# Kernel optimization log

Hardware: AMD Instinct MI355X
Metric: run time of the kernel (lower is better)

## Reference

```python
import jax, jax.numpy as jnp
import numpy as np

# Sinabs LIF semantics (norm_input=True default):
#   v[t] = alpha * v[t-1] + (1 - alpha) * x[t],  alpha = exp(-1/tau_mem)
#   spikes = MultiSpike: max(floor(v / threshold), 0)   (default sa.ActivationFunction)
#   reset  = MembraneSubtract: v -= spikes * threshold
# threshold_low=None -> no lower clamp.

TAU_MEM = 20.0
THRESHOLD = 1.0
GRAD_WIDTH = 0.5   # sinabs SingleExponential surrogate defaults
GRAD_SCALE = 1.0

@jax.custom_vjp
def spike_fn(v):
    # MultiSpike: number of threshold crossings this step
    return jnp.maximum(jnp.floor(v / THRESHOLD), 0.0)

def _spike_fwd(v):
    return spike_fn(v), v

def _spike_bwd(v, g):
    # single-exponential surrogate gradient around threshold
    sg = (GRAD_SCALE / GRAD_WIDTH) * jnp.exp(-jnp.abs(v - THRESHOLD) / GRAD_WIDTH)
    return (g * sg,)

spike_fn.defvjp(_spike_fwd, _spike_bwd)

def lif_layer(x):
    # x: [B, T, N] synaptic input; returns spikes [B, T, N]
    alpha = jnp.exp(jnp.asarray(-1.0 / TAU_MEM, dtype=x.dtype))
    one_m = 1.0 - alpha

    def step(v, xt):
        v = alpha * v + one_m * xt
        s = spike_fn(v)
        v = v - s * THRESHOLD  # membrane subtract reset
        return v, s

    v0 = jnp.zeros(x.shape[:1] + x.shape[2:], dtype=x.dtype)  # [B, N]
    _, spikes = jax.lax.scan(step, v0, jnp.swapaxes(x, 0, 1))  # scan over T
    return jnp.swapaxes(spikes, 0, 1)

def setup_inputs() -> dict:
    key = jax.random.key(0)
    k0, k1, k2, k3 = jax.random.split(key, 4)
    B, T, C_IN = 256, 4096, 16
    data = jax.random.normal(k0, (B, T, C_IN), dtype=jnp.float32)
    # nn.Linear(in, out, bias=False) weights are [out, in], kaiming-uniform-ish scale
    w1 = jax.random.normal(k1, (16, 16), dtype=jnp.float32) / np.sqrt(16)
    w2 = jax.random.normal(k2, (32, 16), dtype=jnp.float32) / np.sqrt(16)
    w3 = jax.random.normal(k3, (10, 32), dtype=jnp.float32) / np.sqrt(32)
    return {"data": data, "w1": w1, "w2": w2, "w3": w3}

def reference(data, w1, w2, w3):
    out = jnp.einsum('btc,oc->bto', data, w1)
    out = lif_layer(out)
    out = jnp.einsum('btc,oc->bto', out, w2)
    out = lif_layer(out)
    out = jnp.einsum('btc,oc->bto', out, w3)
    out = lif_layer(out)
    return out
```

## Files before the change

kernel.cpp:

```cpp
#include <hip/hip_runtime.h>
#include <stdint.h>
#include <math.h>

#define T_STEPS 4096
#define BATCH   256
#define NB_BLK  256

__device__ __forceinline__ float lif_step(float& v, float xs, float alpha) {
    float vp = fmaf(alpha, v, xs);
    float fr = vp - floorf(vp);
    float vn = fminf(vp, fr);
    float s  = vp - vn;
    v = vn;
    return s;
}

__device__ __forceinline__ float ubf(uint32_t w, int k) {
    return (float)((w >> (k * 8)) & 0xffu);
}

__device__ __forceinline__ float dot16(const float wr[16],
    float4 c0, float4 c1, float4 c2, float4 c3)
{
    float p0 = fmaf(wr[1], c0.y, wr[0] * c0.x);
    p0 = fmaf(wr[2], c0.z, p0);  p0 = fmaf(wr[3], c0.w, p0);
    float p1 = fmaf(wr[5], c1.y, wr[4] * c1.x);
    p1 = fmaf(wr[6], c1.z, p1);  p1 = fmaf(wr[7], c1.w, p1);
    float p2 = fmaf(wr[9], c2.y, wr[8] * c2.x);
    p2 = fmaf(wr[10], c2.z, p2); p2 = fmaf(wr[11], c2.w, p2);
    float p3 = fmaf(wr[13], c3.y, wr[12] * c3.x);
    p3 = fmaf(wr[14], c3.z, p3); p3 = fmaf(wr[15], c3.w, p3);
    return (p0 + p1) + (p2 + p3);
}

__global__ __launch_bounds__(1024) void fused(
    const float* __restrict__ x, const float* __restrict__ w1,
    const float* __restrict__ w2, const float* __restrict__ w3,
    float* __restrict__ out, uint8_t* __restrict__ s1t,
    uint8_t* __restrict__ s2t,
    float alpha, float one_m, float alpha16)
{
    const int tid = threadIdx.x;
    const int b   = blockIdx.x;

    __shared__ __align__(16) float xbuf[16640];
    __shared__ float   sh_end[NB_BLK][16];
    __shared__ float   sh_m0[NB_BLK][16];
    __shared__ float   sh_m1[NB_BLK][16];
    __shared__ uint8_t sh_badseg[16][NB_BLK];
    __shared__ uint8_t sh_bm1[NB_BLK];
    __shared__ uint8_t sh_bm2[NB_BLK];
    __shared__ int     sh_badch, sh_spike, sh_flag2;

    const int co = tid & 15;
    const int sg = tid >> 4;
    const int wv = tid >> 6;
    const int ln = tid & 63;

    const float* xb = x + (size_t)b * T_STEPS * 16;
    const float4* xq4 = (const float4*)xb;

    float4 stg[4];
#pragma unroll
    for (int q = 0; q < 4; ++q)
        stg[q] = xq4[(wv * 4 + q) * 64 + ln];

    if (tid < 64)        ((uint32_t*)sh_bm1)[tid] = 0u;
    else if (tid < 128)  ((uint32_t*)sh_bm2)[tid - 64] = 0u;
    else if (tid == 128) { sh_badch = 0; sh_spike = 0; sh_flag2 = 0; }

    float4* o4 = (float4*)(out + (size_t)b * T_STEPS * 10);
    float4 z4 = make_float4(0.f, 0.f, 0.f, 0.f);
#pragma unroll
    for (int i = 0; i < 10; ++i) o4[i * 1024 + tid] = z4;

    float wr[16];
#pragma unroll
    for (int i = 0; i < 16; ++i) wr[i] = one_m * w1[co * 16 + i];

    const int sbase = sg * 260;
    const int wbase = (wv * 4) * 260 + ln * 4;

#pragma unroll
    for (int q = 0; q < 4; ++q)
        *(float4*)&xbuf[wbase + q * 260] = stg[q];

#pragma unroll
    for (int k = 0; k < 4; ++k) {
        if (k < 3) {
#pragma unroll
            for (int q = 0; q < 4; ++q)
                stg[q] = xq4[((k + 1) * 64 + wv * 4 + q) * 64 + ln];
        }

        float acc = 0.0f, m0 = -1e30f, m1 = -1e30f, pw = alpha;
#pragma unroll
        for (int j = 0; j < 16; ++j) {
            const float* rp = &xbuf[sbase + j * 16];
            float4 c0 = *(const float4*)(rp + 0);
            float4 c1 = *(const float4*)(rp + 4);
            float4 c2 = *(const float4*)(rp + 8);
            float4 c3 = *(const float4*)(rp + 12);
            float y = dot16(wr, c0, c1, c2, c3);
            acc = fmaf(alpha, acc, y);
            m0  = fmaxf(m0, acc);
            m1  = fmaxf(m1, acc + pw);
            pw *= alpha;
        }
        const int gs = k * 64 + sg;
        sh_end[gs][co] = acc;
        sh_m0[gs][co]  = m0;
        sh_m1[gs][co]  = m1;

        if (k < 3) {
#pragma unroll
            for (int q = 0; q < 4; ++q)
                *(float4*)&xbuf[wbase + q * 260] = stg[q];
        }
    }
    __syncthreads();

    if (tid < 16) {
        const int c = tid;
        float vs = 0.0f;
        int bad = 0;
#pragma unroll 8
        for (int s = 0; s < NB_BLK; ++s) {
            float vsu = fminf(fmaxf(vs + 1e-3f, 0.0f), 1.0f);
            float bound = fmaf(1.0f - vsu, sh_m0[s][c], vsu * sh_m1[s][c]);
            int sb = (bound >= 0.999f) ? 1 : 0;
            sh_badseg[c][s] = (uint8_t)sb;
            bad |= sb;
            vs = fmaf(alpha16, vs, sh_end[s][c]);
        }
        if (bad) atomicOr(&sh_badch, 1 << c);
    }
    __syncthreads();

    const int badmask = sh_badch;
    if (badmask) {
        uint4* sz = (uint4*)(s1t + (size_t)b * 16 * T_STEPS);
#pragma unroll
        for (int i = 0; i < 4; ++i) sz[i * 1024 + tid] = make_uint4(0u,0u,0u,0u);
        __syncthreads();

        int m = badmask;
        for (int i = 0; i < wv; ++i) m &= m - 1;
        if (ln == 0 && m) {
            const int c = __ffs(m) - 1;
            float wc[16];
#pragma unroll
            for (int i = 0; i < 16; ++i) wc[i] = one_m * w1[c * 16 + i];
            uint8_t* op = s1t + ((size_t)b * 16 + c) * T_STEPS;
            float v = 0.0f;
            int any = 0;
            for (int s = 0; s < NB_BLK; ++s) {
                if (!sh_badseg[c][s]) {
                    v = fmaf(alpha16, v, sh_end[s][c]);
                } else {
                    const float4* xr = (const float4*)xb + (size_t)s * 64;
                    uint32_t w[4] = {0u,0u,0u,0u};
#pragma unroll 4
                    for (int j = 0; j < 16; ++j) {
                        float y  = dot16(wc, xr[j*4+0], xr[j*4+1],
                                              xr[j*4+2], xr[j*4+3]);
                        float sp = lif_step(v, y, alpha);
                        w[j >> 2] |= ((uint32_t)(int)sp) << ((j & 3) * 8);
                    }
                    if (w[0] | w[1] | w[2] | w[3]) {
                        *(uint4*)(op + s * 16) = make_uint4(w[0], w[1], w[2], w[3]);
                        sh_bm1[s] = 1;
                        any = 1;
                    }
                }
            }
            if (any) sh_spike = 1;
        }
    }
    __syncthreads();

    if (sh_spike) {
        if (tid < 32) {
            const int c2 = tid;
            float wr2[16];
#pragma unroll
            for (int i = 0; i < 16; ++i) wr2[i] = one_m * w2[c2 * 16 + i];
            const uint8_t* sb1 = s1t + (size_t)b * 16 * T_STEPS;
            uint4* op2 = (uint4*)(s2t + ((size_t)b * 32 + c2) * T_STEPS);
            const uint4* bmv = (const uint4*)sh_bm1;
            uint8_t* bm2p = sh_bm2;
            float v = 0.0f;
            for (int sb = 0; sb < 16; ++sb) {
                uint4 bm = bmv[sb];
                if ((bm.x | bm.y | bm.z | bm.w) == 0u) {
                    if (v != 0.0f) {
                        for (int blk = 0; blk < 16 && v != 0.0f; ++blk) {
#pragma unroll
                            for (int j = 0; j < 16; ++j) v *= alpha;
                        }
                    }
                    continue;
                }
                for (int blk = 0; blk < 16; ++blk) {
                    uint32_t d = (blk < 4) ? bm.x : (blk < 8) ? bm.y
                               : (blk < 12) ? bm.z : bm.w;
                    uint32_t byte = (d >> ((blk & 3) * 8)) & 0xffu;
                    if (byte == 0u) {
                        if (v != 0.0f) {
#pragma unroll
                            for (int j = 0; j < 16; ++j) v *= alpha;
                        }
                        continue;
                    }
                    const int tb = sb * 16 + blk;
                    const int t0 = tb * 16;
                    uint4 S[16];
#pragma unroll
                    for (int c = 0; c < 16; ++c)
                        S[c] = *(const uint4*)(sb1 + (size_t)c * T_STEPS + t0);
                    uint32_t w[4] = {0u, 0u, 0u, 0u};
#pragma unroll
                    for (int j = 0; j < 16; ++j) {
                        float xv[16];
#pragma unroll
                        for (int c = 0; c < 16; ++c) {
                            uint32_t dd = (j < 4) ? S[c].x : (j < 8) ? S[c].y
                                        : (j < 12) ? S[c].z : S[c].w;
                            xv[c] = ubf(dd, j & 3);
                        }
                        float p0 = fmaf(wr2[1], xv[1], wr2[0] * xv[0]);
                        p0 = fmaf(wr2[2], xv[2], p0);   p0 = fmaf(wr2[3], xv[3], p0);
                        float p1 = fmaf(wr2[5], xv[5], wr2[4] * xv[4]);
                        p1 = fmaf(wr2[6], xv[6], p1);   p1 = fmaf(wr2[7], xv[7], p1);
                        float p2 = fmaf(wr2[9], xv[9], wr2[8] * xv[8]);
                        p2 = fmaf(wr2[10], xv[10], p2); p2 = fmaf(wr2[11], xv[11], p2);
                        float p3 = fmaf(wr2[13], xv[13], wr2[12] * xv[12]);
                        p3 = fmaf(wr2[14], xv[14], p3); p3 = fmaf(wr2[15], xv[15], p3);
                        float xs = (p0 + p1) + (p2 + p3);
                        float s = lif_step(v, xs, alpha);
                        w[j >> 2] |= ((uint32_t)(int)s) << ((j & 3) * 8);
                    }
                    op2[tb] = make_uint4(w[0], w[1], w[2], w[3]);
                    if (w[0] | w[1] | w[2] | w[3]) { bm2p[tb] = 1; sh_flag2 = 1; }
                }
            }
        }
        __syncthreads();

        if (sh_flag2 && tid < 16) {
            const int c3 = tid;
            const bool active = (c3 < 10);
            float wr3[32];
#pragma unroll
            for (int i = 0; i < 32; ++i)
                wr3[i] = active ? (one_m * w3[c3 * 32 + i]) : 0.0f;
            const uint8_t* sb2 = s2t + (size_t)b * 32 * T_STEPS;
            const uint4* bmv2 = (const uint4*)sh_bm2;
            float* ob = out + (size_t)b * T_STEPS * 10 + c3;
            float v = 0.0f;
            for (int sb = 0; sb < 16; ++sb) {
                uint4 bm = bmv2[sb];
                if ((bm.x | bm.y | bm.z | bm.w) == 0u) {
                    if (v != 0.0f) {
                        for (int blk = 0; blk < 16 && v != 0.0f; ++blk) {
#pragma unroll
                            for (int j = 0; j < 16; ++j) v *= alpha;
                        }
                    }
                    continue;
                }
                for (int blk = 0; blk < 16; ++blk) {
                    uint32_t d = (blk < 4) ? bm.x : (blk < 8) ? bm.y
                               : (blk < 12) ? bm.z : bm.w;
                    uint32_t byte = (d >> ((blk & 3) * 8)) & 0xffu;
                    if (byte == 0u) {
                        if (v != 0.0f) {
#pragma unroll
                            for (int j = 0; j < 16; ++j) v *= alpha;
                        }
                        continue;
                    }
                    const int t0 = (sb * 16 + blk) * 16;
                    uint4 S[32];
#pragma unroll
                    for (int c = 0; c < 32; ++c)
                        S[c] = *(const uint4*)(sb2 + (size_t)c * T_STEPS + t0);
#pragma unroll
                    for (int j = 0; j < 16; ++j) {
                        float xv[32];
#pragma unroll
                        for (int c = 0; c < 32; ++c) {
                            uint32_t dd = (j < 4) ? S[c].x : (j < 8) ? S[c].y
                                        : (j < 12) ? S[c].z : S[c].w;
                            xv[c] = ubf(dd, j & 3);
                        }
                        float p0 = fmaf(wr3[1], xv[1], wr3[0] * xv[0]);
                        p0 = fmaf(wr3[2],  xv[2],  p0); p0 = fmaf(wr3[3],  xv[3],  p0);
                        p0 = fmaf(wr3[4],  xv[4],  p0); p0 = fmaf(wr3[5],  xv[5],  p0);
                        p0 = fmaf(wr3[6],  xv[6],  p0); p0 = fmaf(wr3[7],  xv[7],  p0);
                        float p1 = fmaf(wr3[9], xv[9], wr3[8] * xv[8]);
                        p1 = fmaf(wr3[10], xv[10], p1); p1 = fmaf(wr3[11], xv[11], p1);
                        p1 = fmaf(wr3[12], xv[12], p1); p1 = fmaf(wr3[13], xv[13], p1);
                        p1 = fmaf(wr3[14], xv[14], p1); p1 = fmaf(wr3[15], xv[15], p1);
                        float p2 = fmaf(wr3[17], xv[17], wr3[16] * xv[16]);
                        p2 = fmaf(wr3[18], xv[18], p2); p2 = fmaf(wr3[19], xv[19], p2);
                        p2 = fmaf(wr3[20], xv[20], p2); p2 = fmaf(wr3[21], xv[21], p2);
                        p2 = fmaf(wr3[22], xv[22], p2); p2 = fmaf(wr3[23], xv[23], p2);
                        float p3 = fmaf(wr3[25], xv[25], wr3[24] * xv[24]);
                        p3 = fmaf(wr3[26], xv[26], p3); p3 = fmaf(wr3[27], xv[27], p3);
                        p3 = fmaf(wr3[28], xv[28], p3); p3 = fmaf(wr3[29], xv[29], p3);
                        p3 = fmaf(wr3[30], xv[30], p3); p3 = fmaf(wr3[31], xv[31], p3);
                        float xs = (p0 + p1) + (p2 + p3);
                        float s = lif_step(v, xs, alpha);
                        if (active && s != 0.0f) ob[(size_t)(t0 + j) * 10] = s;
                    }
                }
            }
        }
    }
}

extern "C" void kernel_launch(void* const* d_in, const int* in_sizes, int n_in,
                              void* d_out, int out_size, void* d_ws, size_t ws_size,
                              hipStream_t stream)
{
    const float* data = (const float*)d_in[0];
    const float* w1   = (const float*)d_in[1];
    const float* w2   = (const float*)d_in[2];
    const float* w3   = (const float*)d_in[3];
    float* out = (float*)d_out;

    uint8_t* ws  = (uint8_t*)d_ws;
    uint8_t* s1t = ws;
    uint8_t* s2t = ws + (16u << 20);

    const float alpha   = expf(-1.0f / 20.0f);
    const float one_m   = 1.0f - alpha;
    const float alpha16 = expf(-16.0f / 20.0f);

    fused<<<BATCH, 1024, 0, stream>>>(data, w1, w2, w3, out, s1t, s2t,
                                      alpha, one_m, alpha16);
}
```

Baseline: 165.2 us.

## Certify layer-1 quiescence per 4-step segment with per-thread register loads

Layer-1 screening now works on 4-step segments instead of 16-step blocks. Each thread loads its own 64 floats straight into registers, computes all 16 channels and packs fp16 max bounds with the end value into shared memory. This replaces the staged LDS buffer and shared-memory transposes. The serial certification scan is split across 8 groups per channel, each warmed up over 40 previous segments, and bad segments are kept as bitmasks. The finer granularity means fewer steps get recomputed exactly, but fp16 bounds and the truncated warm-up could misjudge a segment near the threshold.

```diff
diff --git a/kernel.cpp b/kernel.cpp
--- a/kernel.cpp
+++ b/kernel.cpp
@@ -1,10 +1,13 @@
 #include <hip/hip_runtime.h>
+#include <hip/hip_fp16.h>
 #include <stdint.h>
 #include <math.h>
 
 #define T_STEPS 4096
 #define BATCH   256
 #define NB_BLK  256
+#define NSEG    1024
+#define EPITCH  1025
 
 __device__ __forceinline__ float lif_step(float& v, float xs, float alpha) {
     float vp = fmaf(alpha, v, xs);
@@ -33,37 +36,30 @@
     return (p0 + p1) + (p2 + p3);
 }
 
-__global__ __launch_bounds__(1024) void fused(
+__global__ __launch_bounds__(1024, 4) void fused(
     const float* __restrict__ x, const float* __restrict__ w1,
     const float* __restrict__ w2, const float* __restrict__ w3,
     float* __restrict__ out, uint8_t* __restrict__ s1t,
     uint8_t* __restrict__ s2t,
-    float alpha, float one_m, float alpha16)
+    float alpha, float one_m, float alpha4)
 {
     const int tid = threadIdx.x;
     const int b   = blockIdx.x;
-
-    __shared__ __align__(16) float xbuf[16640];
-    __shared__ float   sh_end[NB_BLK][16];
-    __shared__ float   sh_m0[NB_BLK][16];
-    __shared__ float   sh_m1[NB_BLK][16];
-    __shared__ uint8_t sh_badseg[16][NB_BLK];
-    __shared__ uint8_t sh_bm1[NB_BLK];
-    __shared__ uint8_t sh_bm2[NB_BLK];
-    __shared__ int     sh_badch, sh_spike, sh_flag2;
-
-    const int co = tid & 15;
-    const int sg = tid >> 4;
-    const int wv = tid >> 6;
-    const int ln = tid & 63;
+    const int wv  = tid >> 6;
+    const int ln  = tid & 63;
+
+    __shared__ float2   sh_cert[16][EPITCH];
+    __shared__ uint32_t sh_badseg[16][NSEG / 32];
+    __shared__ uint8_t  sh_bm1[NB_BLK];
+    __shared__ uint8_t  sh_bm2[NB_BLK];
+    __shared__ int      sh_badch, sh_spike, sh_flag2;
 
     const float* xb = x + (size_t)b * T_STEPS * 16;
     const float4* xq4 = (const float4*)xb;
 
-    float4 stg[4];
-#pragma unroll
-    for (int q = 0; q < 4; ++q)
-        stg[q] = xq4[(wv * 4 + q) * 64 + ln];
+    float4 xr[16];
+#pragma unroll
+    for (int q = 0; q < 16; ++q) xr[q] = xq4[tid * 16 + q];
 
     if (tid < 64)        ((uint32_t*)sh_bm1)[tid] = 0u;
     else if (tid < 128)  ((uint32_t*)sh_bm2)[tid - 64] = 0u;
@@ -74,64 +70,50 @@
 #pragma unroll
     for (int i = 0; i < 10; ++i) o4[i * 1024 + tid] = z4;
 
-    float wr[16];
-#pragma unroll
-    for (int i = 0; i < 16; ++i) wr[i] = one_m * w1[co * 16 + i];
-
-    const int sbase = sg * 260;
-    const int wbase = (wv * 4) * 260 + ln * 4;
-
-#pragma unroll
-    for (int q = 0; q < 4; ++q)
-        *(float4*)&xbuf[wbase + q * 260] = stg[q];
-
-#pragma unroll
-    for (int k = 0; k < 4; ++k) {
-        if (k < 3) {
-#pragma unroll
-            for (int q = 0; q < 4; ++q)
-                stg[q] = xq4[((k + 1) * 64 + wv * 4 + q) * 64 + ln];
-        }
-
+#pragma unroll 2
+    for (int c = 0; c < 16; ++c) {
+        float wc[16];
+#pragma unroll
+        for (int i = 0; i < 16; ++i) wc[i] = w1[c * 16 + i];
         float acc = 0.0f, m0 = -1e30f, m1 = -1e30f, pw = alpha;
 #pragma unroll
-        for (int j = 0; j < 16; ++j) {
-            const float* rp = &xbuf[sbase + j * 16];
-            float4 c0 = *(const float4*)(rp + 0);
-            float4 c1 = *(const float4*)(rp + 4);
-            float4 c2 = *(const float4*)(rp + 8);
-            float4 c3 = *(const float4*)(rp + 12);
-            float y = dot16(wr, c0, c1, c2, c3);
-            acc = fmaf(alpha, acc, y);
+        for (int j = 0; j < 4; ++j) {
+            float y = dot16(wc, xr[j*4+0], xr[j*4+1], xr[j*4+2], xr[j*4+3]);
+            acc = fmaf(alpha, acc, one_m * y);
             m0  = fmaxf(m0, acc);
             m1  = fmaxf(m1, acc + pw);
             pw *= alpha;
         }
-        const int gs = k * 64 + sg;
-        sh_end[gs][co] = acc;
-        sh_m0[gs][co]  = m0;
-        sh_m1[gs][co]  = m1;
-
-        if (k < 3) {
-#pragma unroll
-            for (int q = 0; q < 4; ++q)
-                *(float4*)&xbuf[wbase + q * 260] = stg[q];
-        }
+        unsigned short h0 = __half_as_ushort(__float2half(m0 + 1e-3f));
+        unsigned short h1 = __half_as_ushort(__float2half(m1 + 1e-3f));
+        uint32_t enc = ((uint32_t)h1 << 16) | (uint32_t)h0;
+        sh_cert[c][tid] = make_float2(acc, __uint_as_float(enc));
     }
     __syncthreads();
 
-    if (tid < 16) {
-        const int c = tid;
+    if (tid < 128) {
+        const int c  = tid & 15;
+        const int e8 = tid >> 4;
+        const int s0 = e8 * 128;
         float vs = 0.0f;
+        if (e8 > 0) {
+#pragma unroll 8
+            for (int s = s0 - 40; s < s0; ++s)
+                vs = fmaf(alpha4, vs, sh_cert[c][s].x);
+        }
+        uint32_t bw = 0;
         int bad = 0;
 #pragma unroll 8
-        for (int s = 0; s < NB_BLK; ++s) {
+        for (int s = s0; s < s0 + 128; ++s) {
+            float2 ct = sh_cert[c][s];
+            uint32_t enc = __float_as_uint(ct.y);
+            float m0v = __half2float(__ushort_as_half((unsigned short)(enc & 0xffffu)));
+            float m1v = __half2float(__ushort_as_half((unsigned short)(enc >> 16)));
             float vsu = fminf(fmaxf(vs + 1e-3f, 0.0f), 1.0f);
-            float bound = fmaf(1.0f - vsu, sh_m0[s][c], vsu * sh_m1[s][c]);
-            int sb = (bound >= 0.999f) ? 1 : 0;
-            sh_badseg[c][s] = (uint8_t)sb;
-            bad |= sb;
-            vs = fmaf(alpha16, vs, sh_end[s][c]);
+            float bound = fmaf(1.0f - vsu, m0v, vsu * m1v);
+            if (!(bound < 0.999f)) { bw |= 1u << (s & 31); bad = 1; }
+            if ((s & 31) == 31) { sh_badseg[c][s >> 5] = bw; bw = 0; }
+            vs = fmaf(alpha4, vs, ct.x);
         }
         if (bad) atomicOr(&sh_badch, 1 << c);
     }
@@ -150,27 +132,38 @@
             const int c = __ffs(m) - 1;
             float wc[16];
 #pragma unroll
-            for (int i = 0; i < 16; ++i) wc[i] = one_m * w1[c * 16 + i];
+            for (int i = 0; i < 16; ++i) wc[i] = w1[c * 16 + i];
             uint8_t* op = s1t + ((size_t)b * 16 + c) * T_STEPS;
             float v = 0.0f;
             int any = 0;
-            for (int s = 0; s < NB_BLK; ++s) {
-                if (!sh_badseg[c][s]) {
-                    v = fmaf(alpha16, v, sh_end[s][c]);
+            for (int w32 = 0; w32 < 32; ++w32) {
+                uint32_t bwv = sh_badseg[c][w32];
+                const int sb = w32 * 32;
+                if (bwv == 0u) {
+#pragma unroll 8
+                    for (int q = 0; q < 32; ++q)
+                        v = fmaf(alpha4, v, sh_cert[c][sb + q].x);
                 } else {
-                    const float4* xr = (const float4*)xb + (size_t)s * 64;
-                    uint32_t w[4] = {0u,0u,0u,0u};
-#pragma unroll 4
-                    for (int j = 0; j < 16; ++j) {
-                        float y  = dot16(wc, xr[j*4+0], xr[j*4+1],
-                                              xr[j*4+2], xr[j*4+3]);
-                        float sp = lif_step(v, y, alpha);
-                        w[j >> 2] |= ((uint32_t)(int)sp) << ((j & 3) * 8);
-                    }
-                    if (w[0] | w[1] | w[2] | w[3]) {
-                        *(uint4*)(op + s * 16) = make_uint4(w[0], w[1], w[2], w[3]);
-                        sh_bm1[s] = 1;
-                        any = 1;
+                    for (int q = 0; q < 32; ++q) {
+                        const int s = sb + q;
+                        if (!((bwv >> q) & 1u)) {
+                            v = fmaf(alpha4, v, sh_cert[c][s].x);
+                            continue;
+                        }
+                        const float4* xr2 = xq4 + (size_t)s * 16;
+                        uint32_t sw = 0u;
+#pragma unroll
+                        for (int j = 0; j < 4; ++j) {
+                            float y = dot16(wc, xr2[j*4+0], xr2[j*4+1],
+                                                 xr2[j*4+2], xr2[j*4+3]);
+                            float sp = lif_step(v, one_m * y, alpha);
+                            sw |= ((uint32_t)(int)sp) << (j * 8);
+                        }
+                        if (sw) {
+                            *(uint32_t*)(op + s * 4) = sw;
+                            sh_bm1[s >> 2] = 1;
+                            any = 1;
+                        }
                     }
                 }
             }
@@ -188,7 +181,6 @@
             const uint8_t* sb1 = s1t + (size_t)b * 16 * T_STEPS;
             uint4* op2 = (uint4*)(s2t + ((size_t)b * 32 + c2) * T_STEPS);
             const uint4* bmv = (const uint4*)sh_bm1;
-            uint8_t* bm2p = sh_bm2;
             float v = 0.0f;
             for (int sb = 0; sb < 16; ++sb) {
                 uint4 bm = bmv[sb];
@@ -241,7 +233,7 @@
                         w[j >> 2] |= ((uint32_t)(int)s) << ((j & 3) * 8);
                     }
                     op2[tb] = make_uint4(w[0], w[1], w[2], w[3]);
-                    if (w[0] | w[1] | w[2] | w[3]) { bm2p[tb] = 1; sh_flag2 = 1; }
+                    if (w[0] | w[1] | w[2] | w[3]) { sh_bm2[tb] = 1; sh_flag2 = 1; }
                 }
             }
         }
@@ -334,10 +326,10 @@
     uint8_t* s1t = ws;
     uint8_t* s2t = ws + (16u << 20);
 
-    const float alpha   = expf(-1.0f / 20.0f);
-    const float one_m   = 1.0f - alpha;
-    const float alpha16 = expf(-16.0f / 20.0f);
+    const float alpha  = expf(-1.0f / 20.0f);
+    const float one_m  = 1.0f - alpha;
+    const float alpha4 = expf(-4.0f / 20.0f);
 
     fused<<<BATCH, 1024, 0, stream>>>(data, w1, w2, w3, out, s1t, s2t,
-                                      alpha, one_m, alpha16);
-}
+                                      alpha, one_m, alpha4);
+}
```

Measured after the change: 244.6 us. 1.48x slower.
